# Optimization experiments

Hardware: AMD Instinct MI355X
Metric: run time of the kernel (lower is better)

The kernel has to match this reference:

```python
import jax, jax.numpy as jnp
import numpy as np
from jax import lax


def _trig_expand(x, gridsize):
    # x: [B,C,H,W] -> cos/sin of k*x, each [B,C,H,W,G], k = 1..G
    k = jnp.arange(1, gridsize + 1, dtype=x.dtype)
    xe = x[..., None] * k
    return jnp.cos(xe), jnp.sin(xe)


def _fold_act(t):
    # [B,C,H,W,G] -> [B,C*G,H,W]: grid dim is fully contracted by the conv3d
    # (kernel depth == input depth, no depth padding), so fold it into channels.
    B, C, H, W, G = t.shape
    return t.transpose(0, 1, 4, 2, 3).reshape(B, C * G, H, W)


def _fold_w(w):
    # [O,I,kh,kw,G] -> [O,I*G,kh,kw]
    O, I, kh, kw, G = w.shape
    return w.transpose(0, 1, 4, 2, 3).reshape(O, I * G, kh, kw)


def conv_fourier_kan(x, coeffs, bias, padding, stride=1):
    # coeffs: [2, O, I, k, k, G]; equivalent to torch: pad cos/sin with zeros on
    # H,W then conv3d -> same as 2D conv with zero padding on folded channels.
    G = coeffs.shape[-1]
    c, s = _trig_expand(x, G)

    def conv2d(t, w):
        return lax.conv_general_dilated(
            _fold_act(t), _fold_w(w),
            window_strides=(stride, stride),
            padding=((padding, padding), (padding, padding)),
            dimension_numbers=('NCHW', 'OIHW', 'NCHW'))

    y = conv2d(c, coeffs[0]) + conv2d(s, coeffs[1])
    return y + bias  # bias: [1,O,1,1]


def maxpool2(x):
    return lax.reduce_window(x, -jnp.inf, lax.max, (1, 1, 2, 2), (1, 1, 2, 2), 'VALID')


def naive_fourier_kan(x, coeffs, bias):
    # x: [B,D], coeffs: [2,O,D,G], bias: [1,O]
    G = coeffs.shape[-1]
    k = jnp.arange(1, G + 1, dtype=x.dtype)
    xe = x[:, :, None] * k  # [B,D,G]
    y = jnp.einsum('bdg,odg->bo', jnp.cos(xe), coeffs[0])
    y = y + jnp.einsum('bdg,odg->bo', jnp.sin(xe), coeffs[1])
    return y + bias


def setup_inputs() -> dict:
    key = jax.random.key(0)
    ks = jax.random.split(key, 5)

    def xavier(k, shape):
        fan = np.prod(shape[2:]) * (shape[1] + shape[0])
        bound = float(np.sqrt(6.0 / max(fan, 1)))
        return jax.random.uniform(k, shape, jnp.float32, -bound, bound)

    x = jax.random.normal(ks[0], (256, 1, 28, 28), dtype=jnp.float32)
    return {
        'x': x,
        'c1_coeffs': xavier(ks[1], (2, 13, 1, 5, 5, 5)),
        'c1_bias': jnp.zeros((1, 13, 1, 1), jnp.float32),
        'c2_coeffs': xavier(ks[2], (2, 21, 13, 13, 13, 8)),
        'c2_bias': jnp.zeros((1, 21, 1, 1), jnp.float32),
        'fk1_coeffs': xavier(ks[3], (2, 89, 21 * 7 * 7, 13)),
        'fk1_bias': jnp.zeros((1, 89), jnp.float32),
        'fk2_coeffs': xavier(ks[4], (2, 10, 89, 8)),
        'fk2_bias': jnp.zeros((1, 10), jnp.float32),
    }


def reference(x, c1_coeffs, c1_bias, c2_coeffs, c2_bias,
              fk1_coeffs, fk1_bias, fk2_coeffs, fk2_bias):
    h = conv_fourier_kan(x, c1_coeffs, c1_bias, padding=2)    # [B,13,28,28]
    h = maxpool2(h)                                           # [B,13,14,14]
    h = conv_fourier_kan(h, c2_coeffs, c2_bias, padding=6)    # [B,21,14,14]
    h = maxpool2(h)                                           # [B,21,7,7]
    h = h.reshape(h.shape[0], -1)                             # [B,1029]
    h = naive_fourier_kan(h, fk1_coeffs, fk1_bias)            # [B,89]
    return naive_fourier_kan(h, fk2_coeffs, fk2_bias)         # [B,10]
```

## Files before the change

kernel.cpp:

```cpp
#include <hip/hip_runtime.h>
#include <hip/hip_bf16.h>

typedef _Float16 f16;
typedef f16  f16x4 __attribute__((ext_vector_type(4)));
typedef f16  f16x8 __attribute__((ext_vector_type(8)));
typedef float f32x4 __attribute__((ext_vector_type(4)));
typedef float f32x16 __attribute__((ext_vector_type(16)));

static constexpr size_t TP_OFF = 0;
static constexpr size_t TP_BYTES = (size_t)256 * 26 * 196 * 8 * 2;
static constexpr size_t WB_OFF = TP_OFF + TP_BYTES;
static constexpr size_t WB_BYTES = (size_t)2197 * 64 * 8 * 2;
static constexpr size_t WF_OFF = WB_OFF + WB_BYTES;
static constexpr size_t WF_BYTES = (size_t)33 * 26 * 6 * 64 * 8 * 2;
static constexpr size_t W1_OFF = WF_OFF + WF_BYTES;
static constexpr size_t W1_BYTES = (size_t)39 * 64 * 8 * 2;
static constexpr size_t PP_OFF = W1_OFF + ((W1_BYTES + 255) & ~size_t(255));
static constexpr size_t PP_BYTES = (size_t)2 * 256 * 7 * 32 * 32 * 4;
static constexpr size_t H2_OFF = PP_OFF + PP_BYTES;
static constexpr size_t H2_BYTES = (size_t)256 * 1029 * 4;
static constexpr size_t P3_OFF = H2_OFF + H2_BYTES;

static constexpr int NCH = 33;

__device__ __forceinline__ void prep_wb_body(const float* __restrict__ w2,
                                             f16* __restrict__ Wb2, int bid) {
    int idx = bid * 256 + threadIdx.x;
    if (idx >= 2197 * 64) return;
    int l = idx & 63; int frag = idx >> 6;
    int kx = frag % 13; int t2 = frag / 13;
    int ky = t2 % 13; int cg = t2 / 13;
    int o = l & 31;
    f16x8 v;
#pragma unroll
    for (int i = 0; i < 8; ++i) {
        float wv = 0.f;
        if (o < 21) {
            int ch = cg * 16 + (l >> 5) * 8 + i;
            int c2 = ch / 104, rr = ch % 104, ii = rr >> 3, gg = rr & 7;
            wv = w2[(size_t)(c2 * 21 + o) * 17576 + ii * 1352 + ky * 104 + kx * 8 + gg];
        }
        v[i] = (f16)wv;
    }
    *(f16x8*)&Wb2[(size_t)idx * 8] = v;
}

__device__ __forceinline__ void prep_wf_body(char* smem,
                                             const float* __restrict__ wf1,
                                             f16* __restrict__ Wf1b, int sub) {
    f16 (*Wl)[48 * 32] = (f16(*)[48 * 32])smem;
    int oseg = sub & 1, c = (sub >> 1) & 1, ks = sub >> 2;
    int o0 = oseg * 48;
    int tid = threadIdx.x;
    for (int e = tid; e < 48 * 32; e += 256) {
        int orel = e >> 5, dl = e & 31;
        int o = o0 + orel, d = ks * 32 + dl;
        if (o < 89 && d < 1029) {
            const float* p = wf1 + ((size_t)(c * 89 + o) * 1029 + d) * 13;
#pragma unroll
            for (int g = 0; g < 13; ++g) Wl[g][e] = (f16)p[g];
        } else {
#pragma unroll
            for (int g = 0; g < 13; ++g) Wl[g][e] = (f16)0;
        }
    }
    __syncthreads();
    for (int t = tid; t < 48 * 13 * 4; t += 256) {
        int koct = t & 3; int q = t >> 2; int g = q % 13; int orel = q / 13;
        int o = o0 + orel;
        f16x8 v;
#pragma unroll
        for (int i = 0; i < 8; ++i) v[i] = Wl[g][orel * 32 + koct * 8 + i];
        int l = koct * 16 + (o & 15);
        int nt = o >> 4;
        *(f16x8*)&Wf1b[(((size_t)ks * 26 + c * 13 + g) * 6 + nt) * 512 + (size_t)l * 8] = v;
    }
}

__device__ __forceinline__ void prep_w1_body(const float* __restrict__ w1,
                                             f16* __restrict__ Wb1, int sub) {
    int idx = sub * 256 + threadIdx.x;
    if (idx >= 39 * 64) return;
    int l = idx & 63; int q = idx >> 6;
    int pass = q / 13, kc = q % 13;
    int o = l & 15;
    f16x8 v;
#pragma unroll
    for (int i = 0; i < 8; ++i) {
        int kk = (l >> 4) * 8 + i;
        int tap = 2 * kc + (kk >> 4);
        int j = kk & 15;
        f16 out = (f16)0;
        if (tap < 25 && j < 10 && o < 13) {
            int c = j / 5, g = j % 5;
            int ky = tap / 5, kx = tap - 5 * ky;
            float wv = w1[c * 1625 + o * 125 + ky * 25 + kx * 5 + g];
            f16 hi = (f16)wv;
            out = (pass == 2) ? (f16)(wv - (float)hi) : hi;
        }
        v[i] = out;
    }
    *(f16x8*)&Wb1[(size_t)idx * 8] = v;
}

__global__ __launch_bounds__(256) void k_front(const float* __restrict__ w1,
                                               const float* __restrict__ w2,
                                               const float* __restrict__ wf1,
                                               f16* __restrict__ Wb2,
                                               f16* __restrict__ Wf1b,
                                               f16* __restrict__ Wb1) {
    __shared__ __align__(16) char smem[40960];
    int bid = blockIdx.x;
    if (bid < 553)      prep_wb_body(w2, Wb2, bid);
    else if (bid < 685) prep_wf_body(smem, wf1, Wf1b, bid - 553);
    else                prep_w1_body(w1, Wb1, bid - 685);
}

__global__ __launch_bounds__(256) void k_conv1m(const float* __restrict__ x,
                                                const float* __restrict__ b1,
                                                const f16* __restrict__ Wb1,
                                                f16* __restrict__ Tpre) {
    __shared__ f16 tH[640 * 16];
    __shared__ f16 tL[640 * 16];
    __shared__ float bl[16];
    const int bid = blockIdx.x;
    const int b = bid >> 1, h2 = bid & 1;
    const int base = h2 * 14;
    const int tid = threadIdx.x;
    if (tid < 16) bl[tid] = (tid < 13) ? b1[tid] : 0.f;
    for (int i = tid; i < 640; i += 256) {
        f16x8 z = {};
        *(f16x8*)&tH[i * 16] = z; *(f16x8*)&tH[i * 16 + 8] = z;
        *(f16x8*)&tL[i * 16] = z; *(f16x8*)&tL[i * 16 + 8] = z;
    }
    __syncthreads();
    for (int s = tid; s < 560; s += 256) {
        int r = s / 28, ix = s % 28;
        int iy = base + r - 2;
        if ((unsigned)iy < 28u) {
            float v = x[(size_t)b * 784 + iy * 28 + ix];
            float s1, c1; __sincosf(v, &s1, &c1);
            float cg[5], sg[5];
            float ck = c1, sk = s1, ckm = 1.f, skm = 0.f;
#pragma unroll
            for (int g = 0; g < 5; ++g) {
                cg[g] = ck; sg[g] = sk;
                float cn = 2.f * c1 * ck - ckm, sn = 2.f * c1 * sk - skm;
                ckm = ck; ck = cn; skm = sk; sk = sn;
            }
            f16x8 hA, hB = {}, lA, lB = {};
#pragma unroll
            for (int g = 0; g < 5; ++g) {
                f16 h = (f16)cg[g]; hA[g] = h; lA[g] = (f16)(cg[g] - (float)h);
            }
#pragma unroll
            for (int g = 0; g < 3; ++g) {
                f16 h = (f16)sg[g]; hA[5 + g] = h; lA[5 + g] = (f16)(sg[g] - (float)h);
            }
#pragma unroll
            for (int g = 3; g < 5; ++g) {
                f16 h = (f16)sg[g]; hB[g - 3] = h; lB[g - 3] = (f16)(sg[g] - (float)h);
            }
            int pos = r * 32 + ix + 2;
            *(f16x8*)&tH[pos * 16] = hA; *(f16x8*)&tH[pos * 16 + 8] = hB;
            *(f16x8*)&tL[pos * 16] = lA; *(f16x8*)&tL[pos * 16 + 8] = lB;
        }
    }
    __syncthreads();

    const int l = tid & 63, w = tid >> 6;
    const int col = l & 15, g4 = l >> 4;
    const int tof = g4 >> 1, jh = g4 & 1;
    for (int pi = 0; pi < 2; ++pi) {
        int pl = w + 4 * pi;
        if (pl >= 7) break;
        f32x4 acc[4] = {};
#pragma unroll 1
        for (int pass = 0; pass < 3; ++pass) {
            const f16* pa = (pass == 1) ? tL : tH;
#pragma unroll
            for (int kc = 0; kc < 13; ++kc) {
                f16x8 bf = *(const f16x8*)&Wb1[((size_t)(pass * 13 + kc) * 64 + l) * 8];
                int tap = 2 * kc + tof;
                int ky = tap / 5, kx = tap - 5 * ky;
#pragma unroll
                for (int yy = 0; yy < 2; ++yy)
#pragma unroll
                    for (int hh = 0; hh < 2; ++hh) {
                        int pos = (2 * pl + yy + ky) * 32 + hh * 14 + col + kx;
                        f16x8 a = *(const f16x8*)&pa[pos * 16 + jh * 8];
                        acc[yy * 2 + hh] = __builtin_amdgcn_mfma_f32_16x16x32_f16(a, bf, acc[yy * 2 + hh], 0, 0, 0);
                    }
            }
        }
        if (col < 13) {
            int gpy = h2 * 7 + pl;
#pragma unroll
            for (int hh = 0; hh < 2; ++hh)
#pragma unroll
                for (int jp = 0; jp < 2; ++jp) {
                    if (g4 == 3 && jp == 1) continue;
                    int px = hh * 7 + 2 * g4 + jp;
                    float m = fmaxf(fmaxf(acc[hh][2 * jp], acc[hh][2 * jp + 1]),
                                    fmaxf(acc[2 + hh][2 * jp], acc[2 + hh][2 * jp + 1]));
                    float hval = m + bl[col];
                    float s1, c1; __sincosf(hval, &s1, &c1);
                    f16x8 vc, vs;
                    float ck = c1, sk = s1, ckm = 1.f, skm = 0.f;
#pragma unroll
                    for (int g = 0; g < 8; ++g) {
                        vc[g] = (f16)ck; vs[g] = (f16)sk;
                        float cn = 2.f * c1 * ck - ckm, sn = 2.f * c1 * sk - skm;
                        ckm = ck; ck = cn; skm = sk; sk = sn;
                    }
                    int p = gpy * 14 + px;
                    *(f16x8*)&Tpre[((size_t)(b * 26 + col) * 196 + p) * 8] = vc;
                    *(f16x8*)&Tpre[((size_t)(b * 26 + 13 + col) * 196 + p) * 8] = vs;
                }
        }
    }
}

template<int PAR>
__device__ __forceinline__ void conv2m_body(const f16* __restrict__ Tpre,
                                            const f16* __restrict__ Wb2,
                                            float* __restrict__ Pp,
                                            f16* Tl, int b) {
    const int tid = threadIdx.x;
    const int l = tid & 63, w = tid >> 6;
    const int oct = l >> 5;
    const int pyb = (l >> 4) & 1;
    const int px = l & 15;

    for (int pos = tid; pos < 1792; pos += 256) {
        int yy2 = pos >> 5, xx = pos & 31;
        int yy = yy2 >> 1;
        if (yy < 6 || yy >= 20 || xx < 6 || xx >= 20) {
            f16x8 z = {};
            *(f16x8*)&Tl[(yy2 * 32 + xx) * 8] = z;
        }
    }

    auto ldT = [&](int cg, int j) -> f16x8 {
        int oc = (j >= 196), p = j - oc * 196;
        return *(const f16x8*)&Tpre[((size_t)(b * 26 + 2 * cg + oc) * 196 + p) * 8];
    };
    auto stT = [&](int j, f16x8 v) {
        int oc = (j >= 196), p = j - oc * 196;
        int y = p / 14, xp = p - y * 14;
        *(f16x8*)&Tl[((((y + 6) * 2 + oc) * 32) + xp + 6) * 8] = v;
    };

    f16x8 pr0 = ldT(0, tid);
    f16x8 pr1;
    if (tid < 136) pr1 = ldT(0, tid + 256);

    f32x16 acc[7] = {};

    for (int cg = 0; cg < 13; ++cg) {
        if (cg) __syncthreads();
        stT(tid, pr0);
        if (tid < 136) stT(tid + 256, pr1);
        __syncthreads();
        if (cg + 1 < 13) {
            pr0 = ldT(cg + 1, tid);
            if (tid < 136) pr1 = ldT(cg + 1, tid + 256);
        }

        const int j0 = (w + cg) & 3;
        for (int kxs = 0; kxs < 4; ++kxs) {
            const int kx = j0 + kxs * 4;
            if (kx > 12) break;
            f16x8 bf[7 - PAR];
#pragma unroll
            for (int t = 0; t < 7 - PAR; ++t) {
                int ky = PAR + 2 * t;
                bf[t] = *(const f16x8*)&Wb2[(((size_t)(cg * 13 + ky) * 13 + kx) * 64 + l) * 8];
            }
            const int xx = px + kx;
#pragma unroll
            for (int kp = 0; kp < 13 - PAR; ++kp) {
                const int yy = PAR + 2 * kp + pyb;
                f16x8 a = *(const f16x8*)&Tl[(((yy * 2 + oct) * 32) + xx) * 8];
#pragma unroll
                for (int t = 0; t < 7 - PAR; ++t) {
                    const int mt = kp - t;
                    if (mt >= 0 && mt <= 6)
                        acc[mt] = __builtin_amdgcn_mfma_f32_32x32x16_f16(a, bf[t], acc[mt], 0, 0, 0);
                }
            }
        }
    }

    __syncthreads();
    float* R = (float*)Tl;
    for (int ph = 0; ph < 4; ++ph) {
        if (w == ph) {
#pragma unroll
            for (int mt = 0; mt < 7; ++mt)
#pragma unroll
                for (int reg = 0; reg < 16; ++reg) {
                    int row = (reg & 3) + 8 * (reg >> 2) + 4 * oct;
                    int idx = (mt * 32 + row) * 32 + (l & 31);
                    float v = acc[mt][reg];
                    if (ph) v += R[idx];
                    R[idx] = v;
                }
        }
        __syncthreads();
    }
    float* P = Pp + (size_t)(PAR * 256 + b) * 7168;
    for (int i = tid; i < 7168; i += 256) P[i] = R[i];
}

__global__ __launch_bounds__(256, 2) void k_conv2m(const f16* __restrict__ Tpre,
                                                   const f16* __restrict__ Wb2,
                                                   float* __restrict__ Pp) {
    __shared__ f16 Tl[28 * 2 * 32 * 8];
    int bid = blockIdx.x;
    int b = bid >> 1;
    if (bid & 1) conv2m_body<1>(Tpre, Wb2, Pp, Tl, b);
    else         conv2m_body<0>(Tpre, Wb2, Pp, Tl, b);
}

__global__ __launch_bounds__(256) void k_pool2(const float* __restrict__ Pp,
                                               const float* __restrict__ b2,
                                               float* __restrict__ h2f) {
    int b = blockIdx.x, tid = threadIdx.x;
    for (int idx = tid; idx < 1029; idx += 256) {
        int o = idx % 21; int r = idx / 21; int px = r % 7; int py = r / 7;
        float mx = -1e30f;
#pragma unroll
        for (int sy = 0; sy < 2; ++sy)
#pragma unroll
            for (int sx = 0; sx < 2; ++sx) {
                int py2 = 2 * py + sy, px2 = 2 * px + sx;
                int mt = py2 >> 1, rr = (py2 & 1) * 16 + px2;
                float v = Pp[(size_t)b * 7168 + (mt * 32 + rr) * 32 + o]
                        + Pp[(size_t)(256 + b) * 7168 + (mt * 32 + rr) * 32 + o];
                mx = fmaxf(mx, v);
            }
        h2f[(size_t)b * 1029 + o * 49 + py * 7 + px] = mx + b2[o];
    }
}

__global__ __launch_bounds__(256) void k_fk1m(const float* __restrict__ h2f,
                                              const f16* __restrict__ Wf1b,
                                              float* __restrict__ P3) {
    __shared__ f16 A[26 * 32 * 32];
    const int bid = blockIdx.x;
    const int mt8 = bid / NCH, ks = bid % NCH;
    const int m0 = mt8 * 32, d0 = ks * 32;
    const int tid = threadIdx.x;
    {
        const int m = tid >> 3, dq = tid & 7;
        float c1v[4], ck[4], sk[4], ckm[4], skm[4];
        bool valid[4];
#pragma unroll
        for (int j = 0; j < 4; ++j) {
            int d = d0 + dq * 4 + j;
            valid[j] = d < 1029;
            float h = valid[j] ? h2f[(size_t)(m0 + m) * 1029 + d] : 0.f;
            float s1, c1; __sincosf(h, &s1, &c1);
            c1v[j] = c1;
            ck[j] = c1; sk[j] = s1; ckm[j] = 1.f; skm[j] = 0.f;
        }
#pragma unroll
        for (int g = 0; g < 13; ++g) {
            f16x4 vc, vs;
#pragma unroll
            for (int j = 0; j < 4; ++j) {
                vc[j] = valid[j] ? (f16)ck[j] : (f16)0;
                vs[j] = valid[j] ? (f16)sk[j] : (f16)0;
                float cn = 2.f * c1v[j] * ck[j] - ckm[j];
                float sn = 2.f * c1v[j] * sk[j] - skm[j];
                ckm[j] = ck[j]; ck[j] = cn; skm[j] = sk[j]; sk[j] = sn;
            }
            *(f16x4*)&A[g * 1024 + m * 32 + dq * 4] = vc;
            *(f16x4*)&A[(13 + g) * 1024 + m * 32 + dq * 4] = vs;
        }
    }
    __syncthreads();
    const int w = tid >> 6, l = tid & 63;
    const int mt = w >> 1, ntg = (w & 1) * 3;
    f32x4 acc[3] = {};
    for (int kstep = 0; kstep < 26; ++kstep) {
        f16x8 a = *(const f16x8*)&A[kstep * 1024 + (mt * 16 + (l & 15)) * 32 + (l >> 4) * 8];
#pragma unroll
        for (int j = 0; j < 3; ++j) {
            f16x8 bv = *(const f16x8*)&Wf1b[((((size_t)ks * 26 + kstep) * 6 + ntg + j) * 64 + l) * 8];
            acc[j] = __builtin_amdgcn_mfma_f32_16x16x32_f16(a, bv, acc[j], 0, 0, 0);
        }
    }
    const int o_base = (l & 15);
#pragma unroll
    for (int j = 0; j < 3; ++j) {
        int o = (ntg + j) * 16 + o_base;
        if (o < 89) {
#pragma unroll
            for (int jj = 0; jj < 4; ++jj) {
                int m = m0 + mt * 16 + (l >> 4) * 4 + jj;
                P3[((size_t)ks * 256 + m) * 89 + o] = acc[j][jj];
            }
        }
    }
}

__global__ __launch_bounds__(128) void k_fk2(const float* __restrict__ P3,
                                             const float* __restrict__ bias1,
                                             const float* __restrict__ wf2,
                                             const float* __restrict__ bias2,
                                             float* __restrict__ out) {
    __shared__ float2 tcs2[89][8];
    __shared__ float part[80];
    int b = blockIdx.x, tid = threadIdx.x;
    if (tid < 89) {
        float v = bias1[tid];
        for (int ks = 0; ks < NCH; ++ks)
            v += P3[((size_t)ks * 256 + b) * 89 + tid];
#pragma unroll
        for (int g = 0; g < 8; ++g) {
            float s, c; __sincosf(v * (float)(g + 1), &s, &c);
            tcs2[tid][g] = make_float2(c, s);
        }
    }
    __syncthreads();
    if (tid < 80) {
        int o = tid >> 3, g = tid & 7;
        float s = 0.f;
        for (int d = 0; d < 89; ++d) {
            float2 tv = tcs2[d][g];
            s = fmaf(tv.x, wf2[((size_t)o * 89 + d) * 8 + g],
                fmaf(tv.y, wf2[7120 + ((size_t)o * 89 + d) * 8 + g], s));
        }
        part[tid] = s;
    }
    __syncthreads();
    if (tid < 10) {
        float v = bias2[tid];
#pragma unroll
        for (int g = 0; g < 8; ++g) v += part[tid * 8 + g];
        out[b * 10 + tid] = v;
    }
}

extern "C" void kernel_launch(void* const* d_in, const int* in_sizes, int n_in,
                              void* d_out, int out_size, void* d_ws, size_t ws_size,
                              hipStream_t stream) {
    const float* x   = (const float*)d_in[0];
    const float* w1  = (const float*)d_in[1];
    const float* b1  = (const float*)d_in[2];
    const float* w2  = (const float*)d_in[3];
    const float* b2  = (const float*)d_in[4];
    const float* wf1 = (const float*)d_in[5];
    const float* bf1 = (const float*)d_in[6];
    const float* wf2 = (const float*)d_in[7];
    const float* bf2v = (const float*)d_in[8];

    char* ws  = (char*)d_ws;
    f16*   Tpre = (f16*)(ws + TP_OFF);
    f16*   Wb2  = (f16*)(ws + WB_OFF);
    f16*   Wf1b = (f16*)(ws + WF_OFF);
    f16*   Wb1  = (f16*)(ws + W1_OFF);
    float* Pp   = (float*)(ws + PP_OFF);
    float* h2f  = (float*)(ws + H2_OFF);
    float* P3   = (float*)(ws + P3_OFF);

    k_front<<<695, 256, 0, stream>>>(w1, w2, wf1, Wb2, Wf1b, Wb1);
    k_conv1m<<<512, 256, 0, stream>>>(x, b1, Wb1, Tpre);
    k_conv2m<<<512, 256, 0, stream>>>(Tpre, Wb2, Pp);
    k_pool2<<<256, 256, 0, stream>>>(Pp, b2, h2f);
    k_fk1m<<<8 * NCH, 256, 0, stream>>>(h2f, Wf1b, P3);
    k_fk2<<<256, 128, 0, stream>>>(P3, bf1, wf2, bf2v, (float*)d_out);
}
```

Before: 177.3 us.

## Read conv2 activations directly from global memory instead of staging in LDS

The conv2 MFMA kernel no longer stages each channel group's padded activation tile into shared memory with per-group barriers. Each wave now takes a flat slice of the 169 (cg,kx) work units and loads A fragments straight from global/L2, masking out-of-bounds padding positions with zeros. This removes the 13 per-channel-group __syncthreads and the LDS zero-fill and copy work, but it turns each A-fragment read into a global load that relies on cache hits, and adds address and predicate math in the inner loop. Shared memory now only holds the fp32 reduction buffer.

```diff
diff --git a/kernel.cpp b/kernel.cpp
--- a/kernel.cpp
+++ b/kernel.cpp
@@ -225,75 +225,48 @@
 __device__ __forceinline__ void conv2m_body(const f16* __restrict__ Tpre,
                                             const f16* __restrict__ Wb2,
                                             float* __restrict__ Pp,
-                                            f16* Tl, int b) {
+                                            float* R, int b) {
+    constexpr int NT  = 7 - PAR;
+    constexpr int NKP = 13 - PAR;
     const int tid = threadIdx.x;
     const int l = tid & 63, w = tid >> 6;
     const int oct = l >> 5;
     const int pyb = (l >> 4) & 1;
     const int px = l & 15;
 
-    for (int pos = tid; pos < 1792; pos += 256) {
-        int yy2 = pos >> 5, xx = pos & 31;
-        int yy = yy2 >> 1;
-        if (yy < 6 || yy >= 20 || xx < 6 || xx >= 20) {
-            f16x8 z = {};
-            *(f16x8*)&Tl[(yy2 * 32 + xx) * 8] = z;
-        }
-    }
-
-    auto ldT = [&](int cg, int j) -> f16x8 {
-        int oc = (j >= 196), p = j - oc * 196;
-        return *(const f16x8*)&Tpre[((size_t)(b * 26 + 2 * cg + oc) * 196 + p) * 8];
-    };
-    auto stT = [&](int j, f16x8 v) {
-        int oc = (j >= 196), p = j - oc * 196;
-        int y = p / 14, xp = p - y * 14;
-        *(f16x8*)&Tl[((((y + 6) * 2 + oc) * 32) + xp + 6) * 8] = v;
-    };
-
-    f16x8 pr0 = ldT(0, tid);
-    f16x8 pr1;
-    if (tid < 136) pr1 = ldT(0, tid + 256);
-
+    const f16* Tb = Tpre + (size_t)b * 26 * 196 * 8;
+    const f16x8 zero = {};
     f32x16 acc[7] = {};
 
-    for (int cg = 0; cg < 13; ++cg) {
-        if (cg) __syncthreads();
-        stT(tid, pr0);
-        if (tid < 136) stT(tid + 256, pr1);
-        __syncthreads();
-        if (cg + 1 < 13) {
-            pr0 = ldT(cg + 1, tid);
-            if (tid < 136) pr1 = ldT(cg + 1, tid + 256);
-        }
-
-        const int j0 = (w + cg) & 3;
-        for (int kxs = 0; kxs < 4; ++kxs) {
-            const int kx = j0 + kxs * 4;
-            if (kx > 12) break;
-            f16x8 bf[7 - PAR];
-#pragma unroll
-            for (int t = 0; t < 7 - PAR; ++t) {
-                int ky = PAR + 2 * t;
-                bf[t] = *(const f16x8*)&Wb2[(((size_t)(cg * 13 + ky) * 13 + kx) * 64 + l) * 8];
-            }
-            const int xx = px + kx;
-#pragma unroll
-            for (int kp = 0; kp < 13 - PAR; ++kp) {
-                const int yy = PAR + 2 * kp + pyb;
-                f16x8 a = *(const f16x8*)&Tl[(((yy * 2 + oct) * 32) + xx) * 8];
-#pragma unroll
-                for (int t = 0; t < 7 - PAR; ++t) {
-                    const int mt = kp - t;
-                    if (mt >= 0 && mt <= 6)
-                        acc[mt] = __builtin_amdgcn_mfma_f32_32x32x16_f16(a, bf[t], acc[mt], 0, 0, 0);
-                }
-            }
-        }
-    }
-
-    __syncthreads();
-    float* R = (float*)Tl;
+#pragma unroll 1
+    for (int u = w; u < 169; u += 4) {
+        const int cg = u / 13, kx = u - cg * 13;
+        f16x8 bf[NT];
+#pragma unroll
+        for (int t = 0; t < NT; ++t) {
+            int ky = PAR + 2 * t;
+            bf[t] = *(const f16x8*)&Wb2[(((size_t)(cg * 13 + ky) * 13 + kx) * 64 + l) * 8];
+        }
+        const int x = px + kx - 6;
+        const bool xok = (unsigned)x < 14u;
+        const f16* Tch = Tb + (size_t)(2 * cg + oct) * 196 * 8;
+#pragma unroll
+        for (int kp = 0; kp < NKP; ++kp) {
+            const int y = PAR + 2 * kp + pyb - 6;
+            const bool ok = xok && ((unsigned)y < 14u);
+            const int p = ok ? (y * 14 + x) : 0;
+            f16x8 a = *(const f16x8*)&Tch[(size_t)p * 8];
+            a = ok ? a : zero;
+#pragma unroll
+            for (int t = 0; t < NT; ++t) {
+                const int mt = kp - t;
+                if (mt >= 0 && mt <= 6)
+                    acc[mt] = __builtin_amdgcn_mfma_f32_32x32x16_f16(a, bf[t], acc[mt], 0, 0, 0);
+            }
+        }
+    }
+
+    __syncthreads();
     for (int ph = 0; ph < 4; ++ph) {
         if (w == ph) {
 #pragma unroll
@@ -316,11 +289,11 @@
 __global__ __launch_bounds__(256, 2) void k_conv2m(const f16* __restrict__ Tpre,
                                                    const f16* __restrict__ Wb2,
                                                    float* __restrict__ Pp) {
-    __shared__ f16 Tl[28 * 2 * 32 * 8];
+    __shared__ float R[7 * 32 * 32];
     int bid = blockIdx.x;
     int b = bid >> 1;
-    if (bid & 1) conv2m_body<1>(Tpre, Wb2, Pp, Tl, b);
-    else         conv2m_body<0>(Tpre, Wb2, Pp, Tl, b);
+    if (bid & 1) conv2m_body<1>(Tpre, Wb2, Pp, R, b);
+    else         conv2m_body<0>(Tpre, Wb2, Pp, R, b);
 }
 
 __global__ __launch_bounds__(256) void k_pool2(const float* __restrict__ Pp,
```

New measurement: 201.8 us. 13.8% more time.

## Fuse pool2 into fk1 prologue and double-buffer two channel groups in conv2

Applied to the files above, without the earlier changes.

The separate max-pool kernel is removed, and fk1 now computes the 2x2 max of the summed conv2 partials plus bias directly while building its trig-expanded A tile. This saves a launch and the h2f round trip. Conv2 now stages two channel groups per barrier pair into a doubled shared buffer, which halves the number of syncs and prefetches two groups ahead. The cost is twice the LDS per block, which may reduce occupancy. Each fk1 block also re-reads the partials with strided gathers.

```diff
diff --git a/kernel.cpp b/kernel.cpp
--- a/kernel.cpp
+++ b/kernel.cpp
@@ -17,9 +17,7 @@
 static constexpr size_t W1_BYTES = (size_t)39 * 64 * 8 * 2;
 static constexpr size_t PP_OFF = W1_OFF + ((W1_BYTES + 255) & ~size_t(255));
 static constexpr size_t PP_BYTES = (size_t)2 * 256 * 7 * 32 * 32 * 4;
-static constexpr size_t H2_OFF = PP_OFF + PP_BYTES;
-static constexpr size_t H2_BYTES = (size_t)256 * 1029 * 4;
-static constexpr size_t P3_OFF = H2_OFF + H2_BYTES;
+static constexpr size_t P3_OFF = PP_OFF + PP_BYTES;
 
 static constexpr int NCH = 33;
 
@@ -226,18 +224,20 @@
                                             const f16* __restrict__ Wb2,
                                             float* __restrict__ Pp,
                                             f16* Tl, int b) {
+    constexpr int NT = 7 - PAR;
     const int tid = threadIdx.x;
     const int l = tid & 63, w = tid >> 6;
     const int oct = l >> 5;
     const int pyb = (l >> 4) & 1;
     const int px = l & 15;
 
-    for (int pos = tid; pos < 1792; pos += 256) {
-        int yy2 = pos >> 5, xx = pos & 31;
+    for (int pos = tid; pos < 2 * 1792; pos += 256) {
+        int r = (pos >= 1792) ? pos - 1792 : pos;
+        int yy2 = r >> 5, xx = r & 31;
         int yy = yy2 >> 1;
         if (yy < 6 || yy >= 20 || xx < 6 || xx >= 20) {
             f16x8 z = {};
-            *(f16x8*)&Tl[(yy2 * 32 + xx) * 8] = z;
+            *(f16x8*)&Tl[pos * 8] = z;
         }
     }
 
@@ -245,48 +245,58 @@
         int oc = (j >= 196), p = j - oc * 196;
         return *(const f16x8*)&Tpre[((size_t)(b * 26 + 2 * cg + oc) * 196 + p) * 8];
     };
-    auto stT = [&](int j, f16x8 v) {
+    auto stT = [&](int buf, int j, f16x8 v) {
         int oc = (j >= 196), p = j - oc * 196;
         int y = p / 14, xp = p - y * 14;
-        *(f16x8*)&Tl[((((y + 6) * 2 + oc) * 32) + xp + 6) * 8] = v;
+        *(f16x8*)&Tl[(buf * 1792 + ((y + 6) * 2 + oc) * 32 + xp + 6) * 8] = v;
     };
 
-    f16x8 pr0 = ldT(0, tid);
-    f16x8 pr1;
-    if (tid < 136) pr1 = ldT(0, tid + 256);
+    f16x8 pa = ldT(0, tid);
+    f16x8 pb = ldT(1, tid);
 
     f32x16 acc[7] = {};
 
-    for (int cg = 0; cg < 13; ++cg) {
-        if (cg) __syncthreads();
-        stT(tid, pr0);
-        if (tid < 136) stT(tid + 256, pr1);
+    for (int cgp = 0; cgp < 13; cgp += 2) {
+        const bool hasB = (cgp + 1 < 13);
+        if (cgp) __syncthreads();
+        stT(0, tid, pa);
+        if (tid < 136) stT(0, tid + 256, ldT(cgp, tid + 256));
+        if (hasB) {
+            stT(1, tid, pb);
+            if (tid < 136) stT(1, tid + 256, ldT(cgp + 1, tid + 256));
+        }
         __syncthreads();
-        if (cg + 1 < 13) {
-            pr0 = ldT(cg + 1, tid);
-            if (tid < 136) pr1 = ldT(cg + 1, tid + 256);
-        }
-
-        const int j0 = (w + cg) & 3;
-        for (int kxs = 0; kxs < 4; ++kxs) {
-            const int kx = j0 + kxs * 4;
-            if (kx > 12) break;
-            f16x8 bf[7 - PAR];
-#pragma unroll
-            for (int t = 0; t < 7 - PAR; ++t) {
-                int ky = PAR + 2 * t;
-                bf[t] = *(const f16x8*)&Wb2[(((size_t)(cg * 13 + ky) * 13 + kx) * 64 + l) * 8];
-            }
-            const int xx = px + kx;
-#pragma unroll
-            for (int kp = 0; kp < 13 - PAR; ++kp) {
-                const int yy = PAR + 2 * kp + pyb;
-                f16x8 a = *(const f16x8*)&Tl[(((yy * 2 + oct) * 32) + xx) * 8];
-#pragma unroll
-                for (int t = 0; t < 7 - PAR; ++t) {
-                    const int mt = kp - t;
-                    if (mt >= 0 && mt <= 6)
-                        acc[mt] = __builtin_amdgcn_mfma_f32_32x32x16_f16(a, bf[t], acc[mt], 0, 0, 0);
+        if (cgp + 2 < 13) {
+            pa = ldT(cgp + 2, tid);
+            if (cgp + 3 < 13) pb = ldT(cgp + 3, tid);
+        }
+
+#pragma unroll
+        for (int s = 0; s < 2; ++s) {
+            if (s == 1 && !hasB) break;
+            const int cg = cgp + s;
+            const f16* Tb = &Tl[s * 1792 * 8];
+            const int j0 = (w + cg) & 3;
+            for (int kxs = 0; kxs < 4; ++kxs) {
+                const int kx = j0 + kxs * 4;
+                if (kx > 12) break;
+                f16x8 bf[NT];
+#pragma unroll
+                for (int t = 0; t < NT; ++t) {
+                    int ky = PAR + 2 * t;
+                    bf[t] = *(const f16x8*)&Wb2[(((size_t)(cg * 13 + ky) * 13 + kx) * 64 + l) * 8];
+                }
+                const int xx = px + kx;
+#pragma unroll
+                for (int kp = 0; kp < 13 - PAR; ++kp) {
+                    const int yy = PAR + 2 * kp + pyb;
+                    f16x8 a = *(const f16x8*)&Tb[(((yy * 2 + oct) * 32) + xx) * 8];
+#pragma unroll
+                    for (int t = 0; t < NT; ++t) {
+                        const int mt = kp - t;
+                        if (mt >= 0 && mt <= 6)
+                            acc[mt] = __builtin_amdgcn_mfma_f32_32x32x16_f16(a, bf[t], acc[mt], 0, 0, 0);
+                    }
                 }
             }
         }
@@ -316,35 +326,15 @@
 __global__ __launch_bounds__(256, 2) void k_conv2m(const f16* __restrict__ Tpre,
                                                    const f16* __restrict__ Wb2,
                                                    float* __restrict__ Pp) {
-    __shared__ f16 Tl[28 * 2 * 32 * 8];
+    __shared__ f16 Tl[2 * 28 * 2 * 32 * 8];
     int bid = blockIdx.x;
     int b = bid >> 1;
     if (bid & 1) conv2m_body<1>(Tpre, Wb2, Pp, Tl, b);
     else         conv2m_body<0>(Tpre, Wb2, Pp, Tl, b);
 }
 
-__global__ __launch_bounds__(256) void k_pool2(const float* __restrict__ Pp,
-                                               const float* __restrict__ b2,
-                                               float* __restrict__ h2f) {
-    int b = blockIdx.x, tid = threadIdx.x;
-    for (int idx = tid; idx < 1029; idx += 256) {
-        int o = idx % 21; int r = idx / 21; int px = r % 7; int py = r / 7;
-        float mx = -1e30f;
-#pragma unroll
-        for (int sy = 0; sy < 2; ++sy)
-#pragma unroll
-            for (int sx = 0; sx < 2; ++sx) {
-                int py2 = 2 * py + sy, px2 = 2 * px + sx;
-                int mt = py2 >> 1, rr = (py2 & 1) * 16 + px2;
-                float v = Pp[(size_t)b * 7168 + (mt * 32 + rr) * 32 + o]
-                        + Pp[(size_t)(256 + b) * 7168 + (mt * 32 + rr) * 32 + o];
-                mx = fmaxf(mx, v);
-            }
-        h2f[(size_t)b * 1029 + o * 49 + py * 7 + px] = mx + b2[o];
-    }
-}
-
-__global__ __launch_bounds__(256) void k_fk1m(const float* __restrict__ h2f,
+__global__ __launch_bounds__(256) void k_fk1m(const float* __restrict__ Pp,
+                                              const float* __restrict__ b2,
                                               const f16* __restrict__ Wf1b,
                                               float* __restrict__ P3) {
     __shared__ f16 A[26 * 32 * 32];
@@ -354,13 +344,30 @@
     const int tid = threadIdx.x;
     {
         const int m = tid >> 3, dq = tid & 7;
+        const int img = m0 + m;
+        const float* P0 = Pp + (size_t)img * 7168;
+        const float* P1 = Pp + (size_t)(256 + img) * 7168;
         float c1v[4], ck[4], sk[4], ckm[4], skm[4];
         bool valid[4];
 #pragma unroll
         for (int j = 0; j < 4; ++j) {
             int d = d0 + dq * 4 + j;
             valid[j] = d < 1029;
-            float h = valid[j] ? h2f[(size_t)(m0 + m) * 1029 + d] : 0.f;
+            float h = 0.f;
+            if (valid[j]) {
+                int o = d / 49, pp = d - o * 49;
+                int py = pp / 7, px = pp - py * 7;
+                float mx = -1e30f;
+#pragma unroll
+                for (int sy = 0; sy < 2; ++sy)
+#pragma unroll
+                    for (int sx = 0; sx < 2; ++sx) {
+                        int py2 = 2 * py + sy, px2 = 2 * px + sx;
+                        int idx = (((py2 >> 1) * 32 + (py2 & 1) * 16 + px2) * 32) + o;
+                        mx = fmaxf(mx, P0[idx] + P1[idx]);
+                    }
+                h = mx + b2[o];
+            }
             float s1, c1; __sincosf(h, &s1, &c1);
             c1v[j] = c1;
             ck[j] = c1; sk[j] = s1; ckm[j] = 1.f; skm[j] = 0.f;
@@ -463,13 +470,11 @@
     f16*   Wf1b = (f16*)(ws + WF_OFF);
     f16*   Wb1  = (f16*)(ws + W1_OFF);
     float* Pp   = (float*)(ws + PP_OFF);
-    float* h2f  = (float*)(ws + H2_OFF);
     float* P3   = (float*)(ws + P3_OFF);
 
     k_front<<<695, 256, 0, stream>>>(w1, w2, wf1, Wb2, Wf1b, Wb1);
     k_conv1m<<<512, 256, 0, stream>>>(x, b1, Wb1, Tpre);
     k_conv2m<<<512, 256, 0, stream>>>(Tpre, Wb2, Pp);
-    k_pool2<<<256, 256, 0, stream>>>(Pp, b2, h2f);
-    k_fk1m<<<8 * NCH, 256, 0, stream>>>(h2f, Wf1b, P3);
+    k_fk1m<<<8 * NCH, 256, 0, stream>>>(Pp, b2, Wf1b, P3);
     k_fk2<<<256, 128, 0, stream>>>(P3, bf1, wf2, bf2v, (float*)d_out);
 }
```

Result: slower. 208.8 us (+17.8%).
